# Performance work log

Measured on AMD Instinct MI355X. Metric: run time of the kernel, lower is better.

The kernel has to match this reference:

```python
import jax, jax.numpy as jnp
import numpy as np

B, SQ, SK, D = 4, 2048, 2048, 1024


def setup_inputs() -> dict:
    key = jax.random.key(0)
    ks = jax.random.split(key, 8)
    s = 1.0 / np.sqrt(D)
    return {
        "input_seq": jax.random.normal(ks[0], (B, SQ, D), jnp.float32),
        "condition_seq": jax.random.normal(ks[1], (B, SK, D), jnp.float32),
        "Wq": jax.random.normal(ks[2], (D, D), jnp.float32) * s,
        "bq": jnp.zeros((D,), jnp.float32),
        "Wk": jax.random.normal(ks[3], (D, D), jnp.float32) * s,
        "bk": jnp.zeros((D,), jnp.float32),
        "Wv": jax.random.normal(ks[4], (D, D), jnp.float32) * s,
        "bv": jnp.zeros((D,), jnp.float32),
    }


def reference(input_seq, condition_seq, Wq, bq, Wk, bk, Wv, bv):
    # Linear projections (torch Linear: x @ W.T + b)
    q = jnp.einsum("bsd,ed->bse", input_seq, Wq) + bq        # [B,SQ,D]
    k = jnp.einsum("btd,ed->bte", condition_seq, Wk) + bk    # [B,SK,D]
    v = jnp.einsum("btd,ed->bte", condition_seq, Wv) + bv    # [B,SK,D]
    # NOTE: original module omits the 1/sqrt(d) scaling — kept faithful.
    scores = jnp.einsum("bse,bte->bst", q, k)                # [B,SQ,SK]
    attn = jax.nn.softmax(scores, axis=-1)
    attended = jnp.einsum("bst,bte->bse", attn, v)           # [B,SQ,D]
    return attended
```

## Files before the change

### kernel.cpp

```cpp
#include <hip/hip_runtime.h>

using f32x4  = __attribute__((ext_vector_type(4))) float;
using bf16x8 = __attribute__((ext_vector_type(8))) __bf16;
using f16x8  = __attribute__((ext_vector_type(8))) _Float16;
using u16x4  = __attribute__((ext_vector_type(4))) unsigned short;
using u16x8  = __attribute__((ext_vector_type(8))) unsigned short;

constexpr int Bb = 4, SQn = 2048, SKn = 2048, Dd = 1024;

__device__ __forceinline__ unsigned fbitsu(float x){ union{float f;unsigned u;}c; c.f=x; return c.u; }
__device__ __forceinline__ float ubitsf(unsigned u){ union{unsigned u;float f;}c; c.u=u; return c.f; }
__device__ __forceinline__ unsigned short hi_trunc(float x){ return (unsigned short)(fbitsu(x)>>16); }
__device__ __forceinline__ unsigned short hi_rne(float x){ unsigned u=fbitsu(x); return (unsigned short)((u + 0x7FFFu + ((u>>16)&1u))>>16); }
__device__ __forceinline__ float from_hi(unsigned short h){ return ubitsf(((unsigned)h)<<16); }
__device__ __forceinline__ unsigned short h_rne(float x){ _Float16 h = (_Float16)x; return __builtin_bit_cast(unsigned short, h); }
__device__ __forceinline__ float h2f(unsigned short u){ return (float)__builtin_bit_cast(_Float16, u); }

template<int DT> __device__ __forceinline__ unsigned short cvt_rne(float x){ return DT ? h_rne(x) : hi_rne(x); }
template<int DT> __device__ __forceinline__ float cvt_f(unsigned short u){ return DT ? h2f(u) : from_hi(u); }

__device__ __forceinline__ f32x4 mfma_bf16(bf16x8 a, bf16x8 b, f32x4 c){
    return __builtin_amdgcn_mfma_f32_16x16x32_bf16(a, b, c, 0, 0, 0);
}
__device__ __forceinline__ f32x4 mfma_f16(u16x8 a, u16x8 b, f32x4 c){
    return __builtin_amdgcn_mfma_f32_16x16x32_f16(
        __builtin_bit_cast(f16x8, a), __builtin_bit_cast(f16x8, b), c, 0, 0, 0);
}
template<int DT>
__device__ __forceinline__ f32x4 mfma_u16(u16x8 a, u16x8 b, f32x4 c){
    if constexpr (DT) return mfma_f16(a, b, c);
    else return __builtin_amdgcn_mfma_f32_16x16x32_bf16(
        __builtin_bit_cast(bf16x8, a), __builtin_bit_cast(bf16x8, b), c, 0, 0, 0);
}

__device__ __forceinline__ void gload16(const void* g, void* l){
    __builtin_amdgcn_global_load_lds(
        (const __attribute__((address_space(1))) unsigned int*)g,
        (__attribute__((address_space(3))) unsigned int*)l, 16, 0, 0);
}

__device__ __forceinline__ void xcd_swz(int& bx, int& by){
    const int nx = gridDim.x, nwg = nx * gridDim.y;
    int l = by * nx + bx;
    l = (l & 7) * (nwg >> 3) + (l >> 3);
    bx = l % nx; by = l / nx;
}

__global__ __launch_bounds__(256)
void prep(const float* __restrict__ x, const float* __restrict__ c,
          const float* __restrict__ Wq, const float* __restrict__ Wk,
          const float* __restrict__ Wv,
          unsigned short* __restrict__ xh, unsigned short* __restrict__ xl,
          unsigned short* __restrict__ ch, unsigned short* __restrict__ cl,
          unsigned short* __restrict__ oq, unsigned short* __restrict__ ok,
          unsigned short* __restrict__ ov,
          int n4, int nw4)
{
    const int total = 2*n4 + 3*nw4;
    const int stride = gridDim.x * 256;
    for (int i = blockIdx.x * 256 + threadIdx.x; i < total; i += stride) {
        if (i < 2*n4) {
            const bool second = (i >= n4);
            const int j = second ? i - n4 : i;
            const float* in = second ? c : x;
            unsigned short* hi = second ? ch : xh;
            unsigned short* lo = second ? cl : xl;
            float a[4]; *(float4*)a = *(const float4*)(in + (size_t)j * 4);
            u16x4 h, l;
#pragma unroll
            for (int r = 0; r < 4; ++r) {
                h[r] = h_rne(a[r]);
                l[r] = h_rne(a[r] - h2f(h[r]));
            }
            *(u16x4*)&hi[(size_t)j * 4] = h;
            *(u16x4*)&lo[(size_t)j * 4] = l;
        } else {
            int j = i - 2*n4;
            const float* src; unsigned short* dst;
            if (j < nw4)          { src = Wq; dst = oq; }
            else if (j < 2*nw4)   { src = Wk; dst = ok; j -= nw4; }
            else                  { src = Wv; dst = ov; j -= 2*nw4; }
            float a[4]; *(float4*)a = *(const float4*)(src + (size_t)j * 4);
            u16x4 h;
#pragma unroll
            for (int r = 0; r < 4; ++r) h[r] = h_rne(a[r]);
            *(u16x4*)&dst[(size_t)j * 4] = h;
        }
    }
}

template<int TERMS, int BM_, int BN_, int KS, int EPI, int DT>
__global__ __launch_bounds__(256, 2)
void gemm_tile(const unsigned short* __restrict__ Ahg, const unsigned short* __restrict__ Alg,
               const unsigned short* __restrict__ Bhg, const unsigned short* __restrict__ Blg,
               const float* __restrict__ bias,
               void* __restrict__ O0v, void* __restrict__ O1v,
               int M, int N, int K, long aBS, long bBS, long oBS)
{
    constexpr int CA = BM_ / 16;
    constexpr int CB = BN_ / 16;
    constexpr int AI = BM_ / 32;
    constexpr int BJ = BN_ / 32;
    static_assert(CA % 4 == 0 && CB % 4 == 0, "chunks divisible by 4 waves");

    __shared__ __align__(16) unsigned short Ash[KS][BM_*32], Bsh[KS][BN_*32];
    __shared__ __align__(16) unsigned short Asl[TERMS>=2?KS:1][TERMS>=2?BM_*32:8];
    __shared__ __align__(16) unsigned short Bsl[TERMS==3?KS:1][TERMS==3?BN_*32:8];

    const int z = blockIdx.z;
    Ahg += (size_t)z * aBS;
    Bhg += (size_t)z * bBS;
    if (TERMS >= 2) Alg += (size_t)z * aBS;
    if (TERMS == 3) Blg += (size_t)z * bBS;

    int bx = blockIdx.x, by = blockIdx.y;
    xcd_swz(bx, by);

    const int tid = threadIdx.x, lane = tid & 63, w = tid >> 6;
    const int wr = (w >> 1) * (BM_/2), wc = (w & 1) * (BN_/2);
    const int lr = lane & 15, lg = lane >> 4;
    const int m0 = by * BM_, n0 = bx * BN_;
    const int rowc = lane >> 2;
    const int colb = (lane & 3) << 4;
    const size_t rsBy = (size_t)K * 2;

    f32x4 acc[AI][BJ] = {};

    for (int k0 = 0; k0 < K; k0 += KS*32) {
#pragma unroll
        for (int s = 0; s < KS; ++s) {
#pragma unroll
            for (int c4 = 0; c4 < CA/4; ++c4) {
                const int c = c4*4 + w;
                const size_t go = (size_t)(m0 + c*16 + rowc) * rsBy + (size_t)(k0 + s*32)*2 + colb;
                gload16((const char*)Ahg + go, (char*)&Ash[s][0] + c*1024);
                if (TERMS >= 2) gload16((const char*)Alg + go, (char*)&Asl[s][0] + c*1024);
            }
#pragma unroll
            for (int c4 = 0; c4 < CB/4; ++c4) {
                const int c = c4*4 + w;
                const size_t go = (size_t)(n0 + c*16 + rowc) * rsBy + (size_t)(k0 + s*32)*2 + colb;
                gload16((const char*)Bhg + go, (char*)&Bsh[s][0] + c*1024);
                if (TERMS == 3) gload16((const char*)Blg + go, (char*)&Bsl[s][0] + c*1024);
            }
        }
        __syncthreads();

#pragma unroll
        for (int kk = 0; kk < KS; ++kk) {
            u16x8 ah[AI], bh[BJ];
#pragma unroll
            for (int i = 0; i < AI; ++i) ah[i] = *(const u16x8*)&Ash[kk][(wr + i*16 + lr)*32 + lg*8];
#pragma unroll
            for (int j = 0; j < BJ; ++j) bh[j] = *(const u16x8*)&Bsh[kk][(wc + j*16 + lr)*32 + lg*8];
            if (TERMS == 3) {
                u16x8 al[AI], bl[BJ];
#pragma unroll
                for (int i = 0; i < AI; ++i) al[i] = *(const u16x8*)&Asl[kk][(wr + i*16 + lr)*32 + lg*8];
#pragma unroll
                for (int j = 0; j < BJ; ++j) bl[j] = *(const u16x8*)&Bsl[kk][(wc + j*16 + lr)*32 + lg*8];
#pragma unroll
                for (int i = 0; i < AI; ++i)
#pragma unroll
                    for (int j = 0; j < BJ; ++j) {
                        acc[i][j] = mfma_u16<DT>(ah[i], bh[j], acc[i][j]);
                        acc[i][j] = mfma_u16<DT>(ah[i], bl[j], acc[i][j]);
                        acc[i][j] = mfma_u16<DT>(al[i], bh[j], acc[i][j]);
                    }
            } else if (TERMS == 2) {
                u16x8 al[AI];
#pragma unroll
                for (int i = 0; i < AI; ++i) al[i] = *(const u16x8*)&Asl[kk][(wr + i*16 + lr)*32 + lg*8];
#pragma unroll
                for (int i = 0; i < AI; ++i)
#pragma unroll
                    for (int j = 0; j < BJ; ++j) {
                        acc[i][j] = mfma_u16<DT>(ah[i], bh[j], acc[i][j]);
                        acc[i][j] = mfma_u16<DT>(al[i], bh[j], acc[i][j]);
                    }
            } else {
#pragma unroll
                for (int i = 0; i < AI; ++i)
#pragma unroll
                    for (int j = 0; j < BJ; ++j)
                        acc[i][j] = mfma_u16<DT>(ah[i], bh[j], acc[i][j]);
            }
        }
        __syncthreads();
    }

    if (EPI == 0) {
        float* C = (float*)O0v + (size_t)z * oBS;
#pragma unroll
        for (int j = 0; j < BJ; ++j) {
            const int col = n0 + wc + j*16 + lr;
#pragma unroll
            for (int i = 0; i < AI; ++i)
#pragma unroll
                for (int r = 0; r < 4; ++r)
                    C[(size_t)(m0 + wr + i*16 + lg*4 + r) * N + col] = acc[i][j][r];
        }
    } else {
        unsigned short* Chi = (unsigned short*)O0v + (size_t)z * oBS;
        unsigned short* Clo = (unsigned short*)O1v + (size_t)z * oBS;
#pragma unroll
        for (int j = 0; j < BJ; ++j) {
            const int col = n0 + wc + j*16 + lr;
            const float bc = (EPI == 2) ? bias[col] : 0.f;
#pragma unroll
            for (int i = 0; i < AI; ++i)
#pragma unroll
                for (int r = 0; r < 4; ++r) {
                    const size_t idx = (size_t)(m0 + wr + i*16 + lg*4 + r) * N + col;
                    const float v = acc[i][j][r] + bc;
                    const unsigned short h = cvt_rne<DT>(v);
                    Chi[idx] = h;
                    Clo[idx] = cvt_rne<DT>(v - cvt_f<DT>(h));
                }
        }
    }
}

__global__ __launch_bounds__(256, 2)
void gemm_kv(const unsigned short* __restrict__ Ahg, const unsigned short* __restrict__ Alg,
             const unsigned short* __restrict__ Wk16, const unsigned short* __restrict__ Wv16,
             const float* __restrict__ bk, const float* __restrict__ bv,
             unsigned short* __restrict__ Kh, unsigned short* __restrict__ Vt,
             int M, int N, int K)
{
    constexpr int BM_ = 128, BN_ = 128, BK_ = 32;
    __shared__ __align__(16) unsigned short Ash[BM_*BK_], Asl[BM_*BK_];
    __shared__ __align__(16) unsigned short Bks[BN_*BK_], Bvs[BN_*BK_];

    int bx = blockIdx.x, by = blockIdx.y;
    xcd_swz(bx, by);

    const int tid = threadIdx.x, lane = tid & 63, w = tid >> 6;
    const int wr = (w >> 1) * 64, wc = (w & 1) * 64;
    const int lr = lane & 15, lg = lane >> 4;
    const int m0 = by * BM_, n0 = bx * BN_;
    const int rowc = lane >> 2;
    const int colb = (lane & 3) << 4;
    const size_t rsBy = (size_t)K * 2;

    f32x4 acck[4][4] = {}, accv[4][4] = {};

    for (int k0 = 0; k0 < K; k0 += BK_) {
#pragma unroll
        for (int c4 = 0; c4 < 2; ++c4) {
            const int c = c4*4 + w;
            const size_t goA = (size_t)(m0 + c*16 + rowc) * rsBy + (size_t)k0*2 + colb;
            gload16((const char*)Ahg + goA, (char*)Ash + c*1024);
            gload16((const char*)Alg + goA, (char*)Asl + c*1024);
            const size_t goB = (size_t)(n0 + c*16 + rowc) * rsBy + (size_t)k0*2 + colb;
            gload16((const char*)Wk16 + goB, (char*)Bks + c*1024);
            gload16((const char*)Wv16 + goB, (char*)Bvs + c*1024);
        }
        __syncthreads();

        u16x8 ah[4], al[4], bf[4];
#pragma unroll
        for (int i = 0; i < 4; ++i) {
            ah[i] = *(const u16x8*)&Ash[(wr + i*16 + lr)*BK_ + lg*8];
            al[i] = *(const u16x8*)&Asl[(wr + i*16 + lr)*BK_ + lg*8];
        }
#pragma unroll
        for (int j = 0; j < 4; ++j) bf[j] = *(const u16x8*)&Bks[(wc + j*16 + lr)*BK_ + lg*8];
#pragma unroll
        for (int i = 0; i < 4; ++i)
#pragma unroll
            for (int j = 0; j < 4; ++j) {
                acck[i][j] = mfma_f16(ah[i], bf[j], acck[i][j]);
                acck[i][j] = mfma_f16(al[i], bf[j], acck[i][j]);
            }
#pragma unroll
        for (int j = 0; j < 4; ++j) bf[j] = *(const u16x8*)&Bvs[(wc + j*16 + lr)*BK_ + lg*8];
#pragma unroll
        for (int i = 0; i < 4; ++i)
#pragma unroll
            for (int j = 0; j < 4; ++j) {
                accv[i][j] = mfma_f16(ah[i], bf[j], accv[i][j]);
                accv[i][j] = mfma_f16(al[i], bf[j], accv[i][j]);
            }
        __syncthreads();
    }

#pragma unroll
    for (int j = 0; j < 4; ++j) {
        const int col = n0 + wc + j*16 + lr;
        const float bck = bk[col], bcv = bv[col];
#pragma unroll
        for (int i = 0; i < 4; ++i) {
            const int row0 = m0 + wr + i*16 + lg*4;
#pragma unroll
            for (int r = 0; r < 4; ++r)
                Kh[(size_t)(row0 + r)*N + col] = h_rne(acck[i][j][r] + bck);
            const int b = row0 >> 11, t0 = row0 & 2047;
            u16x4 pk;
#pragma unroll
            for (int r = 0; r < 4; ++r) pk[r] = h_rne(accv[i][j][r] + bcv);
            *(u16x4*)&Vt[(((size_t)b*Dd + col) << 11) + t0] = pk;
        }
    }
}

template<int TERMS, int EPI>
__global__ __launch_bounds__(256, 2)
void gemm_proj(const float* __restrict__ A, const float* __restrict__ Bm,
               const float* __restrict__ bias,
               unsigned short* __restrict__ O0, unsigned short* __restrict__ O1,
               int M, int N, int K)
{
    constexpr int BM_ = 128, BN_ = 64, BK_ = 32;
    __shared__ __align__(16) unsigned short Ash[BM_*BK_], Bsh[BN_*BK_];
    __shared__ __align__(16) unsigned short Asl[TERMS==3?BM_*BK_:8], Bsl[TERMS==3?BN_*BK_:8];

    const int tid = threadIdx.x, lane = tid & 63, w = tid >> 6;
    const int wr = (w >> 1) * 64, wc = (w & 1) * 32;
    const int lr = lane & 15, lg = lane >> 4;
    const int m0 = blockIdx.y * BM_, n0 = blockIdx.x * BN_;

    f32x4 acc[4][2] = {};

    for (int k0 = 0; k0 < K; k0 += BK_) {
        float4 av[4], bv[2];
#pragma unroll
        for (int u = 0; u < 4; ++u) {
            const int f = u*256 + tid;
            av[u] = *(const float4*)(A + (size_t)(m0 + (f >> 3))*K + k0 + ((f & 7) << 2));
        }
#pragma unroll
        for (int u = 0; u < 2; ++u) {
            const int f = u*256 + tid;
            bv[u] = *(const float4*)(Bm + (size_t)(n0 + (f >> 3))*K + k0 + ((f & 7) << 2));
        }
        __syncthreads();
#pragma unroll
        for (int u = 0; u < 4; ++u) {
            const int f = u*256 + tid;
            const int row = f >> 3, ko = (f & 7) << 2;
            float a4[4]; *(float4*)a4 = av[u];
            u16x4 ah;
            if (TERMS == 3) {
                u16x4 al;
#pragma unroll
                for (int j = 0; j < 4; ++j) { ah[j] = hi_trunc(a4[j]); al[j] = hi_trunc(a4[j] - from_hi(ah[j])); }
                *(u16x4*)&Asl[row*BK_ + ko] = al;
            } else {
#pragma unroll
                for (int j = 0; j < 4; ++j) ah[j] = hi_rne(a4[j]);
            }
            *(u16x4*)&Ash[row*BK_ + ko] = ah;
        }
#pragma unroll
        for (int u = 0; u < 2; ++u) {
            const int f = u*256 + tid;
            const int row = f >> 3, ko = (f & 7) << 2;
            float b4[4]; *(float4*)b4 = bv[u];
            u16x4 bh;
            if (TERMS == 3) {
                u16x4 bl;
#pragma unroll
                for (int j = 0; j < 4; ++j) { bh[j] = hi_trunc(b4[j]); bl[j] = hi_trunc(b4[j] - from_hi(bh[j])); }
                *(u16x4*)&Bsl[row*BK_ + ko] = bl;
            } else {
#pragma unroll
                for (int j = 0; j < 4; ++j) bh[j] = hi_rne(b4[j]);
            }
            *(u16x4*)&Bsh[row*BK_ + ko] = bh;
        }
        __syncthreads();

        bf16x8 ah[4], bh[2];
#pragma unroll
        for (int i = 0; i < 4; ++i) ah[i] = *(const bf16x8*)&Ash[(wr + i*16 + lr)*BK_ + lg*8];
#pragma unroll
        for (int j = 0; j < 2; ++j) bh[j] = *(const bf16x8*)&Bsh[(wc + j*16 + lr)*BK_ + lg*8];
        if (TERMS == 3) {
            bf16x8 al[4], bl[2];
#pragma unroll
            for (int i = 0; i < 4; ++i) al[i] = *(const bf16x8*)&Asl[(wr + i*16 + lr)*BK_ + lg*8];
#pragma unroll
            for (int j = 0; j < 2; ++j) bl[j] = *(const bf16x8*)&Bsl[(wc + j*16 + lr)*BK_ + lg*8];
#pragma unroll
            for (int i = 0; i < 4; ++i)
#pragma unroll
                for (int j = 0; j < 2; ++j) {
                    acc[i][j] = mfma_bf16(ah[i], bh[j], acc[i][j]);
                    acc[i][j] = mfma_bf16(ah[i], bl[j], acc[i][j]);
                    acc[i][j] = mfma_bf16(al[i], bh[j], acc[i][j]);
                }
        } else {
#pragma unroll
            for (int i = 0; i < 4; ++i)
#pragma unroll
                for (int j = 0; j < 2; ++j)
                    acc[i][j] = mfma_bf16(ah[i], bh[j], acc[i][j]);
        }
        __syncthreads();
    }

#pragma unroll
    for (int j = 0; j < 2; ++j) {
        const int col = n0 + wc + j*16 + lr;
        const float bc = bias[col];
#pragma unroll
        for (int i = 0; i < 4; ++i) {
            if (EPI == 0) {
#pragma unroll
                for (int r = 0; r < 4; ++r) {
                    const int row = m0 + wr + i*16 + lg*4 + r;
                    const float v = acc[i][j][r] + bc;
                    const unsigned short h = h_rne(v);
                    O0[(size_t)row*N + col] = h;
                    O1[(size_t)row*N + col] = h_rne(v - h2f(h));
                }
            } else if (EPI == 2) {
#pragma unroll
                for (int r = 0; r < 4; ++r) {
                    const int row = m0 + wr + i*16 + lg*4 + r;
                    O0[(size_t)row*N + col] = h_rne(acc[i][j][r] + bc);
                }
            } else {
                const int row0 = m0 + wr + i*16 + lg*4;
                const int b = row0 >> 11, t0 = row0 & 2047;
                u16x4 pk;
#pragma unroll
                for (int r = 0; r < 4; ++r) pk[r] = h_rne(acc[i][j][r] + bc);
                *(u16x4*)&O0[(((size_t)b*Dd + col) << 11) + t0] = pk;
            }
        }
    }
}

__global__ __launch_bounds__(256)
void softmax_sp(unsigned short* __restrict__ Shi, const unsigned short* __restrict__ Slo)
{
    const int tid = threadIdx.x;
    unsigned short* ph = Shi + (size_t)blockIdx.x * SKn;
    const unsigned short* pl = Slo + (size_t)blockIdx.x * SKn;
    __shared__ float red[8];

    u16x8 h8 = *(const u16x8*)&ph[tid*8];
    u16x8 l8 = *(const u16x8*)&pl[tid*8];
    float v[8];
#pragma unroll
    for (int r = 0; r < 8; ++r) v[r] = h2f(h8[r]) + h2f(l8[r]);

    float m = v[0];
#pragma unroll
    for (int r = 1; r < 8; ++r) m = fmaxf(m, v[r]);
#pragma unroll
    for (int o2 = 32; o2 > 0; o2 >>= 1) m = fmaxf(m, __shfl_down(m, o2));
    if ((tid & 63) == 0) red[tid >> 6] = m;
    __syncthreads();
    m = fmaxf(fmaxf(red[0],red[1]), fmaxf(red[2],red[3]));

    float e[8], s = 0.f;
#pragma unroll
    for (int r = 0; r < 8; ++r) { e[r] = __expf(v[r] - m); s += e[r]; }
#pragma unroll
    for (int o2 = 32; o2 > 0; o2 >>= 1) s += __shfl_down(s, o2);
    if ((tid & 63) == 0) red[4 + (tid >> 6)] = s;
    __syncthreads();
    const float inv = 1.f / ((red[4]+red[5])+(red[6]+red[7]));

    u16x8 p8;
#pragma unroll
    for (int r = 0; r < 8; ++r) p8[r] = h_rne(e[r]*inv);
    *(u16x8*)&ph[tid*8] = p8;
}

extern "C" void kernel_launch(void* const* d_in, const int* in_sizes, int n_in,
                              void* d_out, int out_size, void* d_ws, size_t ws_size,
                              hipStream_t stream)
{
    const float* x  = (const float*)d_in[0];
    const float* c  = (const float*)d_in[1];
    const float* Wq = (const float*)d_in[2];
    const float* bq = (const float*)d_in[3];
    const float* Wk = (const float*)d_in[4];
    const float* bk = (const float*)d_in[5];
    const float* Wv = (const float*)d_in[6];
    const float* bv = (const float*)d_in[7];
    float* out = (float*)d_out;

    const size_t nQ = (size_t)Bb * SQn * Dd;
    const size_t sE = (size_t)SQn * SKn;
    const size_t nW = (size_t)Dd * Dd;
    unsigned short* Qh = (unsigned short*)d_ws;
    unsigned short* Ql = Qh + nQ;
    unsigned short* Kh = Ql + nQ;
    unsigned short* Kl = Kh + nQ;
    unsigned short* Vt = Kl + nQ;
    unsigned short* Shi = Vt + nQ;
    unsigned short* Slo = Shi + (size_t)Bb * sE;

    unsigned short* Wq16 = Kl;
    unsigned short* Wk16 = Kl + nW;
    unsigned short* Wv16 = Kl + 2*nW;

    unsigned short* xh = Shi;
    unsigned short* xl = Shi + nQ;
    unsigned short* ch = Slo;
    unsigned short* cl = Slo + nQ;

    const size_t needB = (size_t)(Shi - Qh) * 2 + (size_t)Bb * sE * 2 * 2;
    const bool batched = ws_size >= needB;

    const dim3 blk(256);

    if (batched) {
        prep<<<dim3(4096), blk, 0, stream>>>(x, c, Wq, Wk, Wv,
                                             xh, xl, ch, cl, Wq16, Wk16, Wv16,
                                             (int)(nQ/4), (int)(nW/4));

        gemm_tile<2,128,128,2,2,1><<<dim3(Dd/128, (Bb*SQn)/128), blk, 0, stream>>>(
            xh, xl, Wq16, nullptr, bq, Qh, Ql, Bb*SQn, Dd, Dd, 0, 0, 0);
        gemm_kv<<<dim3(Dd/128, (Bb*SKn)/128), blk, 0, stream>>>(
            ch, cl, Wk16, Wv16, bk, bv, Kh, Vt, Bb*SKn, Dd, Dd);

        gemm_tile<2,128,128,1,1,1><<<dim3(SKn/128, SQn/128, Bb), blk, 0, stream>>>(
            Qh, Ql, Kh, nullptr, nullptr, Shi, Slo, SQn, SKn, Dd,
            (long)SQn*Dd, (long)SKn*Dd, (long)sE);
        softmax_sp<<<dim3(Bb*SQn), blk, 0, stream>>>(Shi, Slo);
        gemm_tile<1,128,128,2,0,1><<<dim3(Dd/128, SQn/128, Bb), blk, 0, stream>>>(
            Shi, nullptr, Vt, nullptr, nullptr, out, nullptr, SQn, Dd, SKn,
            (long)sE, (long)Dd*SKn, (long)SQn*Dd);
    } else {
        unsigned short* ShiF = Shi;
        unsigned short* SloF = Shi + sE;
        gemm_proj<3,0><<<dim3(Dd/64, (Bb*SQn)/128), blk, 0, stream>>>(x, Wq, bq, Qh, Ql, Bb*SQn, Dd, Dd);
        gemm_proj<3,2><<<dim3(Dd/64, (Bb*SKn)/128), blk, 0, stream>>>(c, Wk, bk, Kh, nullptr, Bb*SKn, Dd, Dd);
        gemm_proj<1,1><<<dim3(Dd/64, (Bb*SKn)/128), blk, 0, stream>>>(c, Wv, bv, Vt, nullptr, Bb*SKn, Dd, Dd);
        for (int b = 0; b < Bb; ++b) {
            const size_t qoff = (size_t)b * SQn * Dd;
            const size_t koff = (size_t)b * SKn * Dd;
            gemm_tile<2,128,64,1,1,1><<<dim3(SKn/64, SQn/128, 1), blk, 0, stream>>>(
                Qh+qoff, Ql+qoff, Kh+koff, nullptr, nullptr, ShiF, SloF, SQn, SKn, Dd, 0, 0, 0);
            softmax_sp<<<dim3(SQn), blk, 0, stream>>>(ShiF, SloF);
            gemm_tile<1,64,64,1,0,1><<<dim3(Dd/64, SQn/64, 1), blk, 0, stream>>>(
                ShiF, nullptr, Vt+(size_t)b*Dd*SKn, nullptr, nullptr, out+qoff, nullptr,
                SQn, Dd, SKn, 0, 0, 0);
        }
    }
}
```

Baseline: 274.2 us.

## Split fused K/V projection into two gemm_tile launches and widen QK tile

Removes the dedicated gemm_kv kernel, which computed K and V together while sharing the A tiles. K and V are now computed by two gemm_tile launches that use new epilogues: EPI 3 writes fp16 K plus bias, and EPI 4 writes transposed fp16 V plus bias. The QK^T score GEMM moves from 128x128 to 128x256 tiles. This trades reading the condition activations twice for the more tuned, probably pipelined, gemm_tile path. The larger score tile raises register and LDS pressure per block.

```diff
diff --git a/kernel.cpp b/kernel.cpp
--- a/kernel.cpp
+++ b/kernel.cpp
@@ -200,7 +200,7 @@
                 for (int r = 0; r < 4; ++r)
                     C[(size_t)(m0 + wr + i*16 + lg*4 + r) * N + col] = acc[i][j][r];
         }
-    } else {
+    } else if (EPI == 1 || EPI == 2) {
         unsigned short* Chi = (unsigned short*)O0v + (size_t)z * oBS;
         unsigned short* Clo = (unsigned short*)O1v + (size_t)z * oBS;
 #pragma unroll
@@ -218,88 +218,33 @@
                     Clo[idx] = cvt_rne<DT>(v - cvt_f<DT>(h));
                 }
         }
-    }
-}
-
-__global__ __launch_bounds__(256, 2)
-void gemm_kv(const unsigned short* __restrict__ Ahg, const unsigned short* __restrict__ Alg,
-             const unsigned short* __restrict__ Wk16, const unsigned short* __restrict__ Wv16,
-             const float* __restrict__ bk, const float* __restrict__ bv,
-             unsigned short* __restrict__ Kh, unsigned short* __restrict__ Vt,
-             int M, int N, int K)
-{
-    constexpr int BM_ = 128, BN_ = 128, BK_ = 32;
-    __shared__ __align__(16) unsigned short Ash[BM_*BK_], Asl[BM_*BK_];
-    __shared__ __align__(16) unsigned short Bks[BN_*BK_], Bvs[BN_*BK_];
-
-    int bx = blockIdx.x, by = blockIdx.y;
-    xcd_swz(bx, by);
-
-    const int tid = threadIdx.x, lane = tid & 63, w = tid >> 6;
-    const int wr = (w >> 1) * 64, wc = (w & 1) * 64;
-    const int lr = lane & 15, lg = lane >> 4;
-    const int m0 = by * BM_, n0 = bx * BN_;
-    const int rowc = lane >> 2;
-    const int colb = (lane & 3) << 4;
-    const size_t rsBy = (size_t)K * 2;
-
-    f32x4 acck[4][4] = {}, accv[4][4] = {};
-
-    for (int k0 = 0; k0 < K; k0 += BK_) {
-#pragma unroll
-        for (int c4 = 0; c4 < 2; ++c4) {
-            const int c = c4*4 + w;
-            const size_t goA = (size_t)(m0 + c*16 + rowc) * rsBy + (size_t)k0*2 + colb;
-            gload16((const char*)Ahg + goA, (char*)Ash + c*1024);
-            gload16((const char*)Alg + goA, (char*)Asl + c*1024);
-            const size_t goB = (size_t)(n0 + c*16 + rowc) * rsBy + (size_t)k0*2 + colb;
-            gload16((const char*)Wk16 + goB, (char*)Bks + c*1024);
-            gload16((const char*)Wv16 + goB, (char*)Bvs + c*1024);
-        }
-        __syncthreads();
-
-        u16x8 ah[4], al[4], bf[4];
-#pragma unroll
-        for (int i = 0; i < 4; ++i) {
-            ah[i] = *(const u16x8*)&Ash[(wr + i*16 + lr)*BK_ + lg*8];
-            al[i] = *(const u16x8*)&Asl[(wr + i*16 + lr)*BK_ + lg*8];
-        }
-#pragma unroll
-        for (int j = 0; j < 4; ++j) bf[j] = *(const u16x8*)&Bks[(wc + j*16 + lr)*BK_ + lg*8];
-#pragma unroll
-        for (int i = 0; i < 4; ++i)
-#pragma unroll
-            for (int j = 0; j < 4; ++j) {
-                acck[i][j] = mfma_f16(ah[i], bf[j], acck[i][j]);
-                acck[i][j] = mfma_f16(al[i], bf[j], acck[i][j]);
-            }
-#pragma unroll
-        for (int j = 0; j < 4; ++j) bf[j] = *(const u16x8*)&Bvs[(wc + j*16 + lr)*BK_ + lg*8];
-#pragma unroll
-        for (int i = 0; i < 4; ++i)
-#pragma unroll
-            for (int j = 0; j < 4; ++j) {
-                accv[i][j] = mfma_f16(ah[i], bf[j], accv[i][j]);
-                accv[i][j] = mfma_f16(al[i], bf[j], accv[i][j]);
-            }
-        __syncthreads();
-    }
-
-#pragma unroll
-    for (int j = 0; j < 4; ++j) {
-        const int col = n0 + wc + j*16 + lr;
-        const float bck = bk[col], bcv = bv[col];
-#pragma unroll
-        for (int i = 0; i < 4; ++i) {
-            const int row0 = m0 + wr + i*16 + lg*4;
-#pragma unroll
-            for (int r = 0; r < 4; ++r)
-                Kh[(size_t)(row0 + r)*N + col] = h_rne(acck[i][j][r] + bck);
-            const int b = row0 >> 11, t0 = row0 & 2047;
-            u16x4 pk;
-#pragma unroll
-            for (int r = 0; r < 4; ++r) pk[r] = h_rne(accv[i][j][r] + bcv);
-            *(u16x4*)&Vt[(((size_t)b*Dd + col) << 11) + t0] = pk;
+    } else if (EPI == 3) {
+        unsigned short* C = (unsigned short*)O0v;
+#pragma unroll
+        for (int j = 0; j < BJ; ++j) {
+            const int col = n0 + wc + j*16 + lr;
+            const float bc = bias[col];
+#pragma unroll
+            for (int i = 0; i < AI; ++i)
+#pragma unroll
+                for (int r = 0; r < 4; ++r)
+                    C[(size_t)(m0 + wr + i*16 + lg*4 + r) * N + col] = h_rne(acc[i][j][r] + bc);
+        }
+    } else {
+        unsigned short* Vt = (unsigned short*)O0v;
+#pragma unroll
+        for (int j = 0; j < BJ; ++j) {
+            const int col = n0 + wc + j*16 + lr;
+            const float bc = bias[col];
+#pragma unroll
+            for (int i = 0; i < AI; ++i) {
+                const int row0 = m0 + wr + i*16 + lg*4;
+                const int b = row0 >> 11, t0 = row0 & 2047;
+                u16x4 pk;
+#pragma unroll
+                for (int r = 0; r < 4; ++r) pk[r] = h_rne(acc[i][j][r] + bc);
+                *(u16x4*)&Vt[(((size_t)b*Dd + col) << 11) + t0] = pk;
+            }
         }
     }
 }
@@ -517,10 +462,12 @@
 
         gemm_tile<2,128,128,2,2,1><<<dim3(Dd/128, (Bb*SQn)/128), blk, 0, stream>>>(
             xh, xl, Wq16, nullptr, bq, Qh, Ql, Bb*SQn, Dd, Dd, 0, 0, 0);
-        gemm_kv<<<dim3(Dd/128, (Bb*SKn)/128), blk, 0, stream>>>(
-            ch, cl, Wk16, Wv16, bk, bv, Kh, Vt, Bb*SKn, Dd, Dd);
-
-        gemm_tile<2,128,128,1,1,1><<<dim3(SKn/128, SQn/128, Bb), blk, 0, stream>>>(
+        gemm_tile<2,128,128,2,3,1><<<dim3(Dd/128, (Bb*SKn)/128), blk, 0, stream>>>(
+            ch, cl, Wk16, nullptr, bk, Kh, nullptr, Bb*SKn, Dd, Dd, 0, 0, 0);
+        gemm_tile<2,128,128,2,4,1><<<dim3(Dd/128, (Bb*SKn)/128), blk, 0, stream>>>(
+            ch, cl, Wv16, nullptr, bv, Vt, nullptr, Bb*SKn, Dd, Dd, 0, 0, 0);
+
+        gemm_tile<2,128,256,1,1,1><<<dim3(SKn/256, SQn/128, Bb), blk, 0, stream>>>(
             Qh, Ql, Kh, nullptr, nullptr, Shi, Slo, SQn, SKn, Dd,
             (long)SQn*Dd, (long)SKn*Dd, (long)sE);
         softmax_sp<<<dim3(Bb*SQn), blk, 0, stream>>>(Shi, Slo);
```

Measured after the change: 283.3 us. 3.3% more time.
